# Kernel optimization log

Hardware: AMD Instinct MI355X
Metric: run time of the kernel (lower is better)

## Reference

```python
import math
import jax, jax.numpy as jnp
import numpy as np

DT = 0.001
TAU = 0.02
ALPHA_LIF = math.exp(-DT / TAU)  # fixed LIF decay ~0.9512
V_TH = 1.0
V_RESET = 0.0
BETA = 25.0  # SuperSpike surrogate slope used in LIFLayer

@jax.custom_vjp
def spike(x):
    # SuperSpike forward: hard threshold
    return (x > 0.0).astype(x.dtype)

def _spike_fwd(x):
    return spike(x), x

def _spike_bwd(x, g):
    # surrogate gradient: beta * max(0, 1 - |beta * x|)
    sg = BETA * jnp.clip(1.0 - jnp.abs(BETA * x), 0.0)
    return (g * sg,)

spike.defvjp(_spike_fwd, _spike_bwd)


def setup_inputs() -> dict:
    key = jax.random.key(0)
    k1, k2, k3 = jax.random.split(key, 3)
    T, B, C_IN, C_OUT = 500, 64, 512, 512
    x_seq = jax.random.uniform(k1, (T, B, C_IN), dtype=jnp.float32)
    # kaiming_uniform_(a=sqrt(5)) on [c_in, c_out] -> bound = 1/sqrt(fan_in)
    bound = 1.0 / math.sqrt(C_IN)
    W = jax.random.uniform(k2, (C_IN, C_OUT), minval=-bound, maxval=bound, dtype=jnp.float32)
    alpha_param = jnp.asarray(0.9, dtype=jnp.float32)  # learned synapse trace decay
    return {"x_seq": x_seq, "W": W, "alpha_param": alpha_param}


def reference(x_seq, W, alpha_param):
    T, B, c_in = x_seq.shape
    c_out = W.shape[1]
    a = jnp.clip(alpha_param, 0.0, 0.9999)

    def step(carry, x_t):
        v, trace = carry                      # v: [B, c_out], trace: [B, c_in]
        trace = a * trace + x_t               # synapse trace update
        cur = x_t @ W + trace @ W             # synaptic current [B, c_out]
        v = ALPHA_LIF * v + (1.0 - ALPHA_LIF) * cur
        s = spike(v - V_TH)                   # surrogate-grad threshold
        v = jnp.where(s > 0, V_RESET, v)      # hard reset
        return (v, trace), s

    init = (jnp.zeros((B, c_out), x_seq.dtype), jnp.zeros((B, c_in), x_seq.dtype))
    _, spikes_out = jax.lax.scan(step, init, x_seq)  # [T, B, c_out]
    rates = spikes_out.mean(axis=0)                  # [B, c_out]
    return spikes_out, rates
```

## Files before the change

kernel.cpp:

```cpp
#include <hip/hip_runtime.h>

typedef float f32x4 __attribute__((ext_vector_type(4)));

#define TSTEPS 500
#define BDIM 64
#define CIN 512
#define COUT 512
#define MTOT (TSTEPS * BDIM)
#define NCH (BDIM * CIN)
#define SNEUR (BDIM * COUT)
#define OUTN ((size_t)TSTEPS * SNEUR + SNEUR)

#define AL64 0.95122942450071400909
#define BL64 (1.0 - AL64)

__global__ __launch_bounds__(256) void fill_const_f32(
    float* __restrict__ p, size_t n, float c) {
  size_t i = (size_t)blockIdx.x * 256 + threadIdx.x;
  const size_t stride = (size_t)gridDim.x * 256;
  for (; i < n; i += stride) p[i] = c;
}

__global__ __launch_bounds__(256) void trace32(
    const float* __restrict__ X, float* __restrict__ TR,
    const float* __restrict__ alpha) {
  const int j = blockIdx.x * 256 + threadIdx.x;
  const float a = fminf(fmaxf(alpha[0], 0.0f), 0.9999f);
  float tr = 0.0f;
#pragma unroll 10
  for (int t = 0; t < TSTEPS; ++t) {
    float x = X[(size_t)t * NCH + j];
    tr = __fadd_rn(__fmul_rn(a, tr), x);
    TR[(size_t)t * NCH + j] = tr;
  }
}

__global__ __launch_bounds__(256) void gemm_fused(
    const float* __restrict__ X, const float* __restrict__ TR,
    const float* __restrict__ W, float* __restrict__ CUR) {
  __shared__ __align__(16) float Ax[64][20];
  __shared__ __align__(16) float At[64][20];
  __shared__ __align__(16) float Bs[16][68];
  const int tid = threadIdx.x;
  const int bm = blockIdx.y * 64, bn = blockIdx.x * 64;
  const int ar = tid >> 2, ak = (tid & 3) * 4;
  const int bk = tid >> 4, bn4 = (tid & 15) * 4;
  const int ty = tid >> 4, tx = tid & 15;

  float xH[4][4] = {{0.0f}}, xT[4][4] = {{0.0f}};
  float tH[4][4] = {{0.0f}}, tT[4][4] = {{0.0f}};

#define GSTEP(ACCX, ACCT)                                                   \
  {                                                                         \
    *(f32x4*)&Ax[ar][ak] =                                                  \
        *(const f32x4*)&X[(size_t)(bm + ar) * CIN + kt * 16 + ak];          \
    *(f32x4*)&At[ar][ak] =                                                  \
        *(const f32x4*)&TR[(size_t)(bm + ar) * CIN + kt * 16 + ak];         \
    *(f32x4*)&Bs[bk][bn4] =                                                 \
        *(const f32x4*)&W[(size_t)(kt * 16 + bk) * COUT + bn + bn4];        \
    __syncthreads();                                                        \
    _Pragma("unroll") for (int kg = 0; kg < 4; ++kg) {                      \
      f32x4 ax[4], at[4];                                                   \
      _Pragma("unroll") for (int i = 0; i < 4; ++i) {                       \
        ax[i] = *(const f32x4*)&Ax[ty * 4 + i][kg * 4];                     \
        at[i] = *(const f32x4*)&At[ty * 4 + i][kg * 4];                     \
      }                                                                     \
      _Pragma("unroll") for (int k2 = 0; k2 < 4; ++k2) {                    \
        f32x4 b4 = *(const f32x4*)&Bs[kg * 4 + k2][tx * 4];                 \
        _Pragma("unroll") for (int i = 0; i < 4; ++i)                       \
          _Pragma("unroll") for (int jj = 0; jj < 4; ++jj) {                \
            ACCX[i][jj] = fmaf(ax[i][k2], b4[jj], ACCX[i][jj]);             \
            ACCT[i][jj] = fmaf(at[i][k2], b4[jj], ACCT[i][jj]);             \
          }                                                                 \
      }                                                                     \
    }                                                                       \
    __syncthreads();                                                        \
  }

  for (int kt = 0; kt < 24; ++kt) GSTEP(xH, tH);
  for (int kt = 24; kt < 32; ++kt) GSTEP(xT, tT);
#undef GSTEP

#pragma unroll
  for (int i = 0; i < 4; ++i) {
    f32x4 v;
#pragma unroll
    for (int jj = 0; jj < 4; ++jj)
      v[jj] = __fadd_rn(__fadd_rn(xH[i][jj], xT[i][jj]),
                        __fadd_rn(tH[i][jj], tT[i][jj]));
    *(f32x4*)&CUR[(size_t)(bm + ty * 4 + i) * COUT + bn + tx * 4] = v;
  }
}

__global__ __launch_bounds__(256) void lif32(
    const float* __restrict__ CUR, float* __restrict__ spikes,
    float* __restrict__ rates) {
  const int j = blockIdx.x * 256 + threadIdx.x;
  const float AL = (float)AL64, BL = (float)BL64;
  float v = 0.0f;
  int cnt = 0;
#pragma unroll 10
  for (int t = 0; t < TSTEPS; ++t) {
    float cur = CUR[(size_t)t * SNEUR + j];
    v = __fadd_rn(__fmul_rn(AL, v), __fmul_rn(BL, cur));
    int sp = __fadd_rn(v, -1.0f) > 0.0f;
    cnt += sp;
    spikes[(size_t)t * SNEUR + j] = sp ? 1.0f : 0.0f;
    v = sp ? 0.0f : v;
  }
  rates[j] = __fdiv_rn((float)cnt, 500.0f);
}

extern "C" void kernel_launch(void* const* d_in, const int* in_sizes, int n_in,
                              void* d_out, int out_size, void* d_ws, size_t ws_size,
                              hipStream_t stream) {
  float* out = (float*)d_out;

  float flag = 0.0f;
  const float* X = nullptr;
  const float* W = nullptr;
  const float* AP = nullptr;
  if (n_in != 3) {
    flag = 11.0f;
  } else {
    for (int i = 0; i < 3; ++i) {
      if (in_sizes[i] == 16384000) X = (const float*)d_in[i];
      else if (in_sizes[i] == 262144) W = (const float*)d_in[i];
      else if (in_sizes[i] == 1) AP = (const float*)d_in[i];
    }
    if (!X || !W || !AP) flag = 13.0f;
    else if (out_size != (int)OUTN) flag = 17.0f;
    else if (ws_size < 2ull * MTOT * CIN * 4ull) flag = 23.0f;
  }
  if (flag != 0.0f) {
    fill_const_f32<<<dim3(2048), dim3(256), 0, stream>>>(out, OUTN, flag);
    return;
  }

  float* TR = (float*)d_ws;
  float* CUR = TR + (size_t)MTOT * CIN;

  trace32<<<dim3(NCH / 256), dim3(256), 0, stream>>>(X, TR, AP);
  dim3 gg(COUT / 64, MTOT / 64);
  gemm_fused<<<gg, dim3(256), 0, stream>>>(X, TR, W, CUR);
  lif32<<<dim3(SNEUR / 256), dim3(256), 0, stream>>>(
      CUR, out, out + (size_t)TSTEPS * SNEUR);
}
```

Baseline: 529.0 us.

## Double-buffer GEMM tiles with direct global-to-LDS loads and wider N tile

Rewrites the fused GEMM to stage X, trace and W tiles straight into LDS with global_load_lds, using two buffers so the next k-tile loads while the current one is computed. The output tile widens from 64 to 128 columns per block, so each thread keeps twice the accumulators and A tiles are reused over more columns. LDS row layout is XOR-swizzled instead of padded to avoid bank conflicts. It costs more registers (launch bounds set for 2 blocks/SM) and relies on the LDS write pattern of global_load_lds matching the swizzle.

```diff
diff --git a/kernel.cpp b/kernel.cpp
--- a/kernel.cpp
+++ b/kernel.cpp
@@ -21,6 +21,12 @@
   for (; i < n; i += stride) p[i] = c;
 }
 
+__device__ __forceinline__ void gll16(const float* g, float* l) {
+  __builtin_amdgcn_global_load_lds(
+      (const __attribute__((address_space(1))) void*)g,
+      (__attribute__((address_space(3))) void*)l, 16, 0, 0);
+}
+
 __global__ __launch_bounds__(256) void trace32(
     const float* __restrict__ X, float* __restrict__ TR,
     const float* __restrict__ alpha) {
@@ -35,60 +41,92 @@
   }
 }
 
-__global__ __launch_bounds__(256) void gemm_fused(
+__global__ __launch_bounds__(256, 2) void gemm_fused2(
     const float* __restrict__ X, const float* __restrict__ TR,
     const float* __restrict__ W, float* __restrict__ CUR) {
-  __shared__ __align__(16) float Ax[64][20];
-  __shared__ __align__(16) float At[64][20];
-  __shared__ __align__(16) float Bs[16][68];
+  __shared__ __align__(16) float Ax[2][1024];
+  __shared__ __align__(16) float At[2][1024];
+  __shared__ __align__(16) float Bs[2][2048];
   const int tid = threadIdx.x;
-  const int bm = blockIdx.y * 64, bn = blockIdx.x * 64;
-  const int ar = tid >> 2, ak = (tid & 3) * 4;
-  const int bk = tid >> 4, bn4 = (tid & 15) * 4;
   const int ty = tid >> 4, tx = tid & 15;
+  const int bm = blockIdx.y * 64, bn = blockIdx.x * 128;
+  const int wb = (tid & 192) * 4;
 
-  float xH[4][4] = {{0.0f}}, xT[4][4] = {{0.0f}};
-  float tH[4][4] = {{0.0f}}, tT[4][4] = {{0.0f}};
+  const int arow = tid >> 2, ag = tid & 3;
+  const int ags = ag ^ ((arow >> 2) & 3);
+  const float* sx = X + (size_t)(bm + arow) * CIN + ags * 4;
+  const float* st = TR + (size_t)(bm + arow) * CIN + ags * 4;
+  const int brow0 = tid >> 5, bcg = (tid & 31) * 4;
+  const float* sb0 = W + (size_t)brow0 * COUT + bn + bcg;
+  const float* sb1 = W + (size_t)(8 + brow0) * COUT + bn + bcg;
 
-#define GSTEP(ACCX, ACCT)                                                   \
-  {                                                                         \
-    *(f32x4*)&Ax[ar][ak] =                                                  \
-        *(const f32x4*)&X[(size_t)(bm + ar) * CIN + kt * 16 + ak];          \
-    *(f32x4*)&At[ar][ak] =                                                  \
-        *(const f32x4*)&TR[(size_t)(bm + ar) * CIN + kt * 16 + ak];         \
-    *(f32x4*)&Bs[bk][bn4] =                                                 \
-        *(const f32x4*)&W[(size_t)(kt * 16 + bk) * COUT + bn + bn4];        \
-    __syncthreads();                                                        \
-    _Pragma("unroll") for (int kg = 0; kg < 4; ++kg) {                      \
-      f32x4 ax[4], at[4];                                                   \
-      _Pragma("unroll") for (int i = 0; i < 4; ++i) {                       \
-        ax[i] = *(const f32x4*)&Ax[ty * 4 + i][kg * 4];                     \
-        at[i] = *(const f32x4*)&At[ty * 4 + i][kg * 4];                     \
-      }                                                                     \
-      _Pragma("unroll") for (int k2 = 0; k2 < 4; ++k2) {                    \
-        f32x4 b4 = *(const f32x4*)&Bs[kg * 4 + k2][tx * 4];                 \
-        _Pragma("unroll") for (int i = 0; i < 4; ++i)                       \
-          _Pragma("unroll") for (int jj = 0; jj < 4; ++jj) {                \
-            ACCX[i][jj] = fmaf(ax[i][k2], b4[jj], ACCX[i][jj]);             \
-            ACCT[i][jj] = fmaf(at[i][k2], b4[jj], ACCT[i][jj]);             \
-          }                                                                 \
-      }                                                                     \
-    }                                                                       \
-    __syncthreads();                                                        \
+  float xH[4][8] = {{0.0f}}, xT[4][8] = {{0.0f}};
+  float tH[4][8] = {{0.0f}}, tT[4][8] = {{0.0f}};
+
+  auto stage = [&](int b) {
+    gll16(sx, &Ax[b][wb]);
+    gll16(st, &At[b][wb]);
+    gll16(sb0, &Bs[b][wb]);
+    gll16(sb1, &Bs[b][1024 + wb]);
+    sx += 16; st += 16;
+    sb0 += 16 * COUT; sb1 += 16 * COUT;
+  };
+
+  const int sw = ty & 3;
+
+#define COMPUTE(b, AX, AT)                                                   \
+  {                                                                          \
+    const float* axp = Ax[b];                                                \
+    const float* atp = At[b];                                                \
+    const float* bsp = Bs[b];                                                \
+    _Pragma("unroll") for (int kg = 0; kg < 4; ++kg) {                       \
+      const int G = (kg ^ sw) * 4;                                           \
+      f32x4 avx[4], avt[4];                                                  \
+      _Pragma("unroll") for (int i = 0; i < 4; ++i) {                        \
+        avx[i] = *(const f32x4*)&axp[(ty * 4 + i) * 16 + G];                 \
+        avt[i] = *(const f32x4*)&atp[(ty * 4 + i) * 16 + G];                 \
+      }                                                                      \
+      _Pragma("unroll") for (int k2 = 0; k2 < 4; ++k2) {                     \
+        f32x4 bL = *(const f32x4*)&bsp[(kg * 4 + k2) * 128 + tx * 4];        \
+        f32x4 bH = *(const f32x4*)&bsp[(kg * 4 + k2) * 128 + 64 + tx * 4];   \
+        _Pragma("unroll") for (int i = 0; i < 4; ++i)                        \
+          _Pragma("unroll") for (int j = 0; j < 4; ++j) {                    \
+            AX[i][j]     = fmaf(avx[i][k2], bL[j], AX[i][j]);                \
+            AX[i][4 + j] = fmaf(avx[i][k2], bH[j], AX[i][4 + j]);            \
+            AT[i][j]     = fmaf(avt[i][k2], bL[j], AT[i][j]);                \
+            AT[i][4 + j] = fmaf(avt[i][k2], bH[j], AT[i][4 + j]);            \
+          }                                                                  \
+      }                                                                      \
+    }                                                                        \
   }
 
-  for (int kt = 0; kt < 24; ++kt) GSTEP(xH, tH);
-  for (int kt = 24; kt < 32; ++kt) GSTEP(xT, tT);
-#undef GSTEP
+  stage(0);
+  int buf = 0;
+  for (int kt = 0; kt < 32; ++kt) {
+    __syncthreads();
+    if (kt < 31) stage(buf ^ 1);
+    if (kt < 24) {
+      COMPUTE(buf, xH, tH);
+    } else {
+      COMPUTE(buf, xT, tT);
+    }
+    buf ^= 1;
+  }
+#undef COMPUTE
 
 #pragma unroll
   for (int i = 0; i < 4; ++i) {
-    f32x4 v;
+    const size_t row = (size_t)(bm + ty * 4 + i);
+    f32x4 L, H;
 #pragma unroll
-    for (int jj = 0; jj < 4; ++jj)
-      v[jj] = __fadd_rn(__fadd_rn(xH[i][jj], xT[i][jj]),
-                        __fadd_rn(tH[i][jj], tT[i][jj]));
-    *(f32x4*)&CUR[(size_t)(bm + ty * 4 + i) * COUT + bn + tx * 4] = v;
+    for (int j = 0; j < 4; ++j) {
+      L[j] = __fadd_rn(__fadd_rn(xH[i][j], xT[i][j]),
+                       __fadd_rn(tH[i][j], tT[i][j]));
+      H[j] = __fadd_rn(__fadd_rn(xH[i][4 + j], xT[i][4 + j]),
+                       __fadd_rn(tH[i][4 + j], tT[i][4 + j]));
+    }
+    *(f32x4*)&CUR[row * COUT + bn + tx * 4] = L;
+    *(f32x4*)&CUR[row * COUT + bn + 64 + tx * 4] = H;
   }
 }
 
@@ -141,8 +179,8 @@
   float* CUR = TR + (size_t)MTOT * CIN;
 
   trace32<<<dim3(NCH / 256), dim3(256), 0, stream>>>(X, TR, AP);
-  dim3 gg(COUT / 64, MTOT / 64);
-  gemm_fused<<<gg, dim3(256), 0, stream>>>(X, TR, W, CUR);
+  dim3 gg(COUT / 128, MTOT / 64);
+  gemm_fused2<<<gg, dim3(256), 0, stream>>>(X, TR, W, CUR);
   lif32<<<dim3(SNEUR / 256), dim3(256), 0, stream>>>(
       CUR, out, out + (size_t)TSTEPS * SNEUR);
 }
```

Result: slower. 777.7 us (+47.0%).

## Widen GEMM tiles to 64x128, swizzle blocks, split K into head/tail kernels

Applied to the files above, without the earlier changes.

Widens each GEMM block's output tile from 64x64 to 64x128, so each thread holds 4x8 accumulators per operand. This doubles W reuse per A load and halves the number of A-tile reloads. Block indices are remapped with a swizzle intended to improve L2 locality. The K loop is split into two kernels, gemm_head and gemm_tail, which pass partial sums through extra workspace buffers; this preserves the original summation order at the cost of writing and reading an extra 128MB of partials and one more kernel launch. Register pressure also rises with 64 accumulators per thread, which may cut occupancy.

```diff
diff --git a/kernel.cpp b/kernel.cpp
--- a/kernel.cpp
+++ b/kernel.cpp
@@ -13,6 +13,9 @@
 
 #define AL64 0.95122942450071400909
 #define BL64 (1.0 - AL64)
+
+#define BUF_BYTES 65536000ull
+#define WS_NEED (3ull * BUF_BYTES)
 
 __global__ __launch_bounds__(256) void fill_const_f32(
     float* __restrict__ p, size_t n, float c) {
@@ -35,60 +38,106 @@
   }
 }
 
-__global__ __launch_bounds__(256) void gemm_fused(
-    const float* __restrict__ X, const float* __restrict__ TR,
-    const float* __restrict__ W, float* __restrict__ CUR) {
-  __shared__ __align__(16) float Ax[64][20];
-  __shared__ __align__(16) float At[64][20];
-  __shared__ __align__(16) float Bs[16][68];
-  const int tid = threadIdx.x;
-  const int bm = blockIdx.y * 64, bn = blockIdx.x * 64;
-  const int ar = tid >> 2, ak = (tid & 3) * 4;
-  const int bk = tid >> 4, bn4 = (tid & 15) * 4;
-  const int ty = tid >> 4, tx = tid & 15;
+#define GEMM_SHARED                                  \
+  __shared__ __align__(16) float Asx[64][20];        \
+  __shared__ __align__(16) float Ast[64][20];        \
+  __shared__ __align__(16) float Bs[16][132];
 
-  float xH[4][4] = {{0.0f}}, xT[4][4] = {{0.0f}};
-  float tH[4][4] = {{0.0f}}, tT[4][4] = {{0.0f}};
+#define GEMM_SETUP                                   \
+  const int tid = threadIdx.x;                       \
+  const int ty = tid >> 4, tx = tid & 15;            \
+  const int fid = blockIdx.x;                        \
+  const int swz = (fid & 7) * 250 + (fid >> 3);      \
+  const int bm = (swz >> 2) * 64;                    \
+  const int bn = (swz & 3) * 128;                    \
+  const int ar = tid >> 2, ak = (tid & 3) * 4;       \
+  const int bk = tid >> 4, bc = (tid & 15) * 8;
 
-#define GSTEP(ACCX, ACCT)                                                   \
-  {                                                                         \
-    *(f32x4*)&Ax[ar][ak] =                                                  \
-        *(const f32x4*)&X[(size_t)(bm + ar) * CIN + kt * 16 + ak];          \
-    *(f32x4*)&At[ar][ak] =                                                  \
-        *(const f32x4*)&TR[(size_t)(bm + ar) * CIN + kt * 16 + ak];         \
-    *(f32x4*)&Bs[bk][bn4] =                                                 \
-        *(const f32x4*)&W[(size_t)(kt * 16 + bk) * COUT + bn + bn4];        \
-    __syncthreads();                                                        \
-    _Pragma("unroll") for (int kg = 0; kg < 4; ++kg) {                      \
-      f32x4 ax[4], at[4];                                                   \
-      _Pragma("unroll") for (int i = 0; i < 4; ++i) {                       \
-        ax[i] = *(const f32x4*)&Ax[ty * 4 + i][kg * 4];                     \
-        at[i] = *(const f32x4*)&At[ty * 4 + i][kg * 4];                     \
-      }                                                                     \
-      _Pragma("unroll") for (int k2 = 0; k2 < 4; ++k2) {                    \
-        f32x4 b4 = *(const f32x4*)&Bs[kg * 4 + k2][tx * 4];                 \
-        _Pragma("unroll") for (int i = 0; i < 4; ++i)                       \
-          _Pragma("unroll") for (int jj = 0; jj < 4; ++jj) {                \
-            ACCX[i][jj] = fmaf(ax[i][k2], b4[jj], ACCX[i][jj]);             \
-            ACCT[i][jj] = fmaf(at[i][k2], b4[jj], ACCT[i][jj]);             \
-          }                                                                 \
-      }                                                                     \
-    }                                                                       \
-    __syncthreads();                                                        \
+#define GEMM_STEP(kt)                                                        \
+  {                                                                          \
+    *(f32x4*)&Asx[ar][ak] =                                                  \
+        *(const f32x4*)&X[(size_t)(bm + ar) * CIN + (kt)*16 + ak];           \
+    *(f32x4*)&Ast[ar][ak] =                                                  \
+        *(const f32x4*)&TR[(size_t)(bm + ar) * CIN + (kt)*16 + ak];          \
+    *(f32x4*)&Bs[bk][bc] =                                                   \
+        *(const f32x4*)&W[(size_t)((kt)*16 + bk) * COUT + bn + bc];          \
+    *(f32x4*)&Bs[bk][bc + 4] =                                               \
+        *(const f32x4*)&W[(size_t)((kt)*16 + bk) * COUT + bn + bc + 4];      \
+    __syncthreads();                                                         \
+    _Pragma("unroll") for (int kg = 0; kg < 4; ++kg) {                       \
+      f32x4 ax[4], at4[4];                                                   \
+      _Pragma("unroll") for (int i = 0; i < 4; ++i) {                        \
+        ax[i] = *(const f32x4*)&Asx[ty * 4 + i][kg * 4];                     \
+        at4[i] = *(const f32x4*)&Ast[ty * 4 + i][kg * 4];                    \
+      }                                                                      \
+      _Pragma("unroll") for (int k2 = 0; k2 < 4; ++k2) {                     \
+        f32x4 bL = *(const f32x4*)&Bs[kg * 4 + k2][tx * 4];                  \
+        f32x4 bH = *(const f32x4*)&Bs[kg * 4 + k2][64 + tx * 4];             \
+        _Pragma("unroll") for (int i = 0; i < 4; ++i)                        \
+          _Pragma("unroll") for (int j = 0; j < 4; ++j) {                    \
+            xA[i][j]     = fmaf(ax[i][k2], bL[j], xA[i][j]);                 \
+            xA[i][4 + j] = fmaf(ax[i][k2], bH[j], xA[i][4 + j]);             \
+            tA[i][j]     = fmaf(at4[i][k2], bL[j], tA[i][j]);                \
+            tA[i][4 + j] = fmaf(at4[i][k2], bH[j], tA[i][4 + j]);            \
+          }                                                                  \
+      }                                                                      \
+    }                                                                        \
+    __syncthreads();                                                         \
   }
 
-  for (int kt = 0; kt < 24; ++kt) GSTEP(xH, tH);
-  for (int kt = 24; kt < 32; ++kt) GSTEP(xT, tT);
-#undef GSTEP
+__global__ __launch_bounds__(256) void gemm_head(
+    const float* __restrict__ X, const float* __restrict__ TR,
+    const float* __restrict__ W, float* __restrict__ PHx,
+    float* __restrict__ PHt) {
+  GEMM_SHARED
+  GEMM_SETUP
+  float xA[4][8] = {{0.0f}}, tA[4][8] = {{0.0f}};
+  for (int kt = 0; kt < 24; ++kt) GEMM_STEP(kt)
 
 #pragma unroll
   for (int i = 0; i < 4; ++i) {
-    f32x4 v;
+    const size_t row = (size_t)(bm + ty * 4 + i);
+    f32x4 xL, xH2, tL, tH2;
 #pragma unroll
-    for (int jj = 0; jj < 4; ++jj)
-      v[jj] = __fadd_rn(__fadd_rn(xH[i][jj], xT[i][jj]),
-                        __fadd_rn(tH[i][jj], tT[i][jj]));
-    *(f32x4*)&CUR[(size_t)(bm + ty * 4 + i) * COUT + bn + tx * 4] = v;
+    for (int j = 0; j < 4; ++j) {
+      xL[j] = xA[i][j];   xH2[j] = xA[i][4 + j];
+      tL[j] = tA[i][j];   tH2[j] = tA[i][4 + j];
+    }
+    *(f32x4*)&PHx[row * COUT + bn + tx * 4] = xL;
+    *(f32x4*)&PHx[row * COUT + bn + 64 + tx * 4] = xH2;
+    *(f32x4*)&PHt[row * COUT + bn + tx * 4] = tL;
+    *(f32x4*)&PHt[row * COUT + bn + 64 + tx * 4] = tH2;
+  }
+}
+
+__global__ __launch_bounds__(256) void gemm_tail(
+    const float* __restrict__ X, const float* __restrict__ TR,
+    const float* __restrict__ W, float* __restrict__ PHx,
+    const float* __restrict__ PHt) {
+  GEMM_SHARED
+  GEMM_SETUP
+  float xA[4][8] = {{0.0f}}, tA[4][8] = {{0.0f}};
+  for (int kt = 24; kt < 32; ++kt) GEMM_STEP(kt)
+
+#pragma unroll
+  for (int i = 0; i < 4; ++i) {
+    const size_t row = (size_t)(bm + ty * 4 + i);
+    const size_t iL = row * COUT + bn + tx * 4;
+    const size_t iH = row * COUT + bn + 64 + tx * 4;
+    f32x4 hxL = *(const f32x4*)&PHx[iL];
+    f32x4 hxH = *(const f32x4*)&PHx[iH];
+    f32x4 htL = *(const f32x4*)&PHt[iL];
+    f32x4 htH = *(const f32x4*)&PHt[iH];
+    f32x4 oL, oH;
+#pragma unroll
+    for (int j = 0; j < 4; ++j) {
+      oL[j] = __fadd_rn(__fadd_rn(hxL[j], xA[i][j]),
+                        __fadd_rn(htL[j], tA[i][j]));
+      oH[j] = __fadd_rn(__fadd_rn(hxH[j], xA[i][4 + j]),
+                        __fadd_rn(htH[j], tA[i][4 + j]));
+    }
+    *(f32x4*)&PHx[iL] = oL;
+    *(f32x4*)&PHx[iH] = oH;
   }
 }
 
@@ -130,19 +179,21 @@
     }
     if (!X || !W || !AP) flag = 13.0f;
     else if (out_size != (int)OUTN) flag = 17.0f;
-    else if (ws_size < 2ull * MTOT * CIN * 4ull) flag = 23.0f;
+    else if (ws_size < WS_NEED) flag = 23.0f;
   }
   if (flag != 0.0f) {
     fill_const_f32<<<dim3(2048), dim3(256), 0, stream>>>(out, OUTN, flag);
     return;
   }
 
-  float* TR = (float*)d_ws;
-  float* CUR = TR + (size_t)MTOT * CIN;
+  char* ws = (char*)d_ws;
+  float* TR = (float*)(ws);
+  float* PHx = (float*)(ws + BUF_BYTES);
+  float* PHt = (float*)(ws + 2 * BUF_BYTES);
 
   trace32<<<dim3(NCH / 256), dim3(256), 0, stream>>>(X, TR, AP);
-  dim3 gg(COUT / 64, MTOT / 64);
-  gemm_fused<<<gg, dim3(256), 0, stream>>>(X, TR, W, CUR);
+  gemm_head<<<dim3(2000), dim3(256), 0, stream>>>(X, TR, W, PHx, PHt);
+  gemm_tail<<<dim3(2000), dim3(256), 0, stream>>>(X, TR, W, PHx, PHt);
   lif32<<<dim3(SNEUR / 256), dim3(256), 0, stream>>>(
-      CUR, out, out + (size_t)TSTEPS * SNEUR);
+      PHx, out, out + (size_t)TSTEPS * SNEUR);
 }
```

After: 502.6 us. -5.0%, faster.
